# Performance work log

Hardware: AMD Instinct MI355X
Metric: run time of the kernel (lower is better)

The kernel has to match this reference:

```python
import jax, jax.numpy as jnp
import numpy as np

P, D_IN, RANK, D_OUT, N = 64, 1024, 64, 1024, 4096


def setup_inputs() -> dict:
    key = jax.random.key(0)
    k1, k2, k3, k4, k5 = jax.random.split(key, 5)
    x = jax.random.normal(k1, (N, D_IN), dtype=jnp.float32)
    pids = jax.random.randint(k2, (N,), 0, P, dtype=jnp.int64)
    U = jax.random.normal(k3, (P, D_IN, RANK), dtype=jnp.float32) * 0.02
    V = jax.random.normal(k4, (P, RANK, D_OUT), dtype=jnp.float32) * 0.02
    bias = jax.random.normal(k5, (D_OUT,), dtype=jnp.float32)
    return {"x": x, "pids": pids, "U": U, "V": V, "bias": bias}


def reference(x, pids, U, V, bias):
    # Equivalent to: for each token n, out[n] = x[n] @ U[pids[n]] @ V[pids[n]] + bias
    # Computed as dense grouped GEMM over all partitions, then row-select by pid
    # (identical math to the masked per-partition loop in the torch module).
    h = jnp.einsum('nd,pdr->pnr', x, U)        # [P, N, R]
    o = jnp.einsum('pnr,pro->pno', h, V)       # [P, N, D_out]
    out = o[pids, jnp.arange(x.shape[0])] + bias  # select each token's own partition
    return out
```

## Files before the change

kernel.cpp:

```cpp
#include <hip/hip_runtime.h>
#include <hip/hip_bf16.h>

#define NP     64
#define D_IN   1024
#define RANK   64
#define D_OUT  1024
#define NTOK   4096
#define TM     64
#define BK     64
#define MT     128
#define KS     8
#define KW     (D_IN / KS)
#define OW     128
#define LDSTR  72
#define BTH    1024

typedef __bf16 bf16x8 __attribute__((ext_vector_type(8)));
typedef float  f32x4  __attribute__((ext_vector_type(4)));

__device__ __forceinline__ unsigned short f2bf(float f) {
    unsigned u = __builtin_bit_cast(unsigned, f);
    u += 0x7FFFu + ((u >> 16) & 1u);
    return (unsigned short)(u >> 16);
}
__device__ __forceinline__ float bf2f(unsigned short s) {
    unsigned u = (unsigned)s << 16;
    return __builtin_bit_cast(float, u);
}
__device__ __forceinline__ bf16x8 pack8(float4 a, float4 b) {
    union { bf16x8 v; unsigned short s[8]; } r;
    r.s[0] = f2bf(a.x); r.s[1] = f2bf(a.y); r.s[2] = f2bf(a.z); r.s[3] = f2bf(a.w);
    r.s[4] = f2bf(b.x); r.s[5] = f2bf(b.y); r.s[6] = f2bf(b.z); r.s[7] = f2bf(b.w);
    return r.v;
}

__device__ __forceinline__ int swz_idx(int outer, int inner) {
    int blk = (inner >> 3) ^ ((outer >> 3) & 7);
    return outer * LDSTR + blk * 8 + (inner & 7);
}

__device__ __forceinline__ void decode_xcd(int b, int& tile, int& slice) {
    int g = b & 7;
    int l = b >> 3;
    slice = l >> 4;
    int m = l & 15;
    tile = (((m >> 1) << 3) | g) * 2 + (m & 1);
}

__global__ __launch_bounds__(BTH) void bucket_kernel(
    const int* __restrict__ pids, int* __restrict__ meta)
{
    __shared__ int counts[NP];
    __shared__ int cursor[NP];
    int tid = threadIdx.x;
    if (tid < NP) counts[tid] = 0;
    __syncthreads();
    for (int i = tid; i < NTOK / 4; i += BTH) {
        int4 pv = reinterpret_cast<const int4*>(pids)[i];
        atomicAdd(&counts[pv.x & (NP - 1)], 1);
        atomicAdd(&counts[pv.y & (NP - 1)], 1);
        atomicAdd(&counts[pv.z & (NP - 1)], 1);
        atomicAdd(&counts[pv.w & (NP - 1)], 1);
    }
    __syncthreads();
    if (tid < 64) {
        int c = counts[tid];
        int ntp = (c + TM - 1) >> 6;
        int sc = c, st = ntp;
        for (int d = 1; d < 64; d <<= 1) {
            int vc = __shfl_up(sc, d);
            int vt = __shfl_up(st, d);
            if (tid >= d) { sc += vc; st += vt; }
        }
        int cbase = sc - c;
        int tb    = st - ntp;
        cursor[tid] = cbase;
        for (int t = 0; t < ntp; ++t) {
            int idx = tb + t;
            int rem = c - t * TM;
            int4 rec = {tid, cbase + t * TM, rem < TM ? rem : TM, 0};
            *reinterpret_cast<int4*>(meta + 16 + 4 * idx) = rec;
        }
        if (tid == 63) meta[0] = st;
    }
    __syncthreads();
    int* bucket = meta + 1024;
    for (int i = tid; i < NTOK / 4; i += BTH) {
        int4 pv = reinterpret_cast<const int4*>(pids)[i];
        bucket[atomicAdd(&cursor[pv.x & (NP - 1)], 1)] = i * 4 + 0;
        bucket[atomicAdd(&cursor[pv.y & (NP - 1)], 1)] = i * 4 + 1;
        bucket[atomicAdd(&cursor[pv.z & (NP - 1)], 1)] = i * 4 + 2;
        bucket[atomicAdd(&cursor[pv.w & (NP - 1)], 1)] = i * 4 + 3;
    }
}

__global__ __launch_bounds__(256, 4) void h_kernel(
    const float* __restrict__ x, const float* __restrict__ U,
    const int* __restrict__ meta, unsigned short* __restrict__ Hpart)
{
    __shared__ __align__(16) unsigned short Us[2][RANK * LDSTR];

    int tile, ks;
    decode_xcd(blockIdx.x, tile, ks);
    int nt = meta[0];
    if (tile >= nt) return;
    int4 ti = *reinterpret_cast<const int4*>(meta + 16 + 4 * tile);
    int p = ti.x, off = ti.y, len = ti.z;

    int tid  = threadIdx.x;
    int lane = tid & 63;
    int w    = tid >> 6;
    int l15  = lane & 15;
    int l4   = lane >> 4;

    int myrow = w * 16 + l15;
    const int* bucket = meta + 1024;
    int t = (myrow < len) ? bucket[off + myrow] : -1;
    bool valid = (t >= 0);
    const float* xrow = x + (size_t)(valid ? t : 0) * D_IN;
    const float* Up = U + (size_t)p * D_IN * RANK;

    int kbeg = ks * KW;
    int kk = tid >> 2;
    int q  = (tid & 3) * 16;

    float4 z{0,0,0,0};
    float4 c0a=z,c0b=z,c0c=z,c0d=z,c1a=z,c1b=z,c1c=z,c1d=z;
    if (valid) {
        const float* xp = xrow + kbeg + l4 * 8;
        c0a = *reinterpret_cast<const float4*>(xp);
        c0b = *reinterpret_cast<const float4*>(xp + 4);
        c0c = *reinterpret_cast<const float4*>(xp + 32);
        c0d = *reinterpret_cast<const float4*>(xp + 36);
        c1a = *reinterpret_cast<const float4*>(xp + 64);
        c1b = *reinterpret_cast<const float4*>(xp + 68);
        c1c = *reinterpret_cast<const float4*>(xp + 96);
        c1d = *reinterpret_cast<const float4*>(xp + 100);
    }

    f32x4 acc[4] = {};

    {
        const float* up = Up + (size_t)(kbeg + kk) * RANK + q;
#pragma unroll
        for (int i = 0; i < 4; ++i) {
            float4 v = *reinterpret_cast<const float4*>(up + i * 4);
            int r = q + i * 4;
            Us[0][swz_idx(r + 0, kk)] = f2bf(v.x);
            Us[0][swz_idx(r + 1, kk)] = f2bf(v.y);
            Us[0][swz_idx(r + 2, kk)] = f2bf(v.z);
            Us[0][swz_idx(r + 3, kk)] = f2bf(v.w);
        }
    }
    __syncthreads();

    float4 u10, u11, u12, u13;
    {
        const float* up = Up + (size_t)(kbeg + BK + kk) * RANK + q;
        u10 = *reinterpret_cast<const float4*>(up);
        u11 = *reinterpret_cast<const float4*>(up + 4);
        u12 = *reinterpret_cast<const float4*>(up + 8);
        u13 = *reinterpret_cast<const float4*>(up + 12);
    }

    {
        bf16x8 a0 = pack8(c0a, c0b);
        bf16x8 a1 = pack8(c0c, c0d);
#pragma unroll
        for (int k2 = 0; k2 < 2; ++k2) {
            int kof = k2 * 32 + l4 * 8;
            bf16x8 a = k2 ? a1 : a0;
#pragma unroll
            for (int ni = 0; ni < 4; ++ni) {
                bf16x8 b = *reinterpret_cast<const bf16x8*>(&Us[0][swz_idx(ni * 16 + l15, kof)]);
                acc[ni] = __builtin_amdgcn_mfma_f32_16x16x32_bf16(a, b, acc[ni], 0, 0, 0);
            }
        }
    }

    {
        float4 vv[4] = {u10, u11, u12, u13};
#pragma unroll
        for (int i = 0; i < 4; ++i) {
            int r = q + i * 4;
            Us[1][swz_idx(r + 0, kk)] = f2bf(vv[i].x);
            Us[1][swz_idx(r + 1, kk)] = f2bf(vv[i].y);
            Us[1][swz_idx(r + 2, kk)] = f2bf(vv[i].z);
            Us[1][swz_idx(r + 3, kk)] = f2bf(vv[i].w);
        }
    }
    __syncthreads();

    {
        bf16x8 a0 = pack8(c1a, c1b);
        bf16x8 a1 = pack8(c1c, c1d);
#pragma unroll
        for (int k2 = 0; k2 < 2; ++k2) {
            int kof = k2 * 32 + l4 * 8;
            bf16x8 a = k2 ? a1 : a0;
#pragma unroll
            for (int ni = 0; ni < 4; ++ni) {
                bf16x8 b = *reinterpret_cast<const bf16x8*>(&Us[1][swz_idx(ni * 16 + l15, kof)]);
                acc[ni] = __builtin_amdgcn_mfma_f32_16x16x32_bf16(a, b, acc[ni], 0, 0, 0);
            }
        }
    }

    unsigned short* hp = Hpart + ((size_t)ks * MT + tile) * (TM * RANK);
#pragma unroll
    for (int ni = 0; ni < 4; ++ni)
#pragma unroll
        for (int j = 0; j < 4; ++j) {
            int row = w * 16 + l4 * 4 + j;
            int col = ni * 16 + l15;
            hp[row * RANK + col] = f2bf(acc[ni][j]);
        }
}

__global__ __launch_bounds__(256, 4) void o_kernel(
    const float* __restrict__ V, const float* __restrict__ bias,
    const int* __restrict__ meta, const unsigned short* __restrict__ Hpart,
    float* __restrict__ out)
{
    __shared__ __align__(16) unsigned short Vs[OW * LDSTR];

    int tile, ocs;
    decode_xcd(blockIdx.x, tile, ocs);
    int oc = ocs * OW;
    int nt = meta[0];
    if (tile >= nt) return;
    int4 ti = *reinterpret_cast<const int4*>(meta + 16 + 4 * tile);
    int p = ti.x, off = ti.y, len = ti.z;

    int tid  = threadIdx.x;
    int lane = tid & 63;
    int w    = tid >> 6;
    int l15  = lane & 15;
    int l4   = lane >> 4;

    const float* Vp = V + (size_t)p * RANK * D_OUT;
    int o4 = (tid & 31) * 4;
    int rb = tid >> 5;
    float4 vv[8];
#pragma unroll
    for (int pass = 0; pass < 8; ++pass) {
        int r = pass * 8 + rb;
        vv[pass] = *reinterpret_cast<const float4*>(&Vp[(size_t)r * D_OUT + oc + o4]);
    }

    size_t hoff = (size_t)tile * (TM * RANK) + (w * 16 + l15) * RANK + l4 * 8;
    float s0[8] = {}, s1[8] = {};
#pragma unroll
    for (int k = 0; k < KS; ++k) {
        const unsigned short* pp = Hpart + (size_t)k * (MT * TM * RANK) + hoff;
        union { int4 i4; unsigned short u[8]; } va, vb;
        va.i4 = *reinterpret_cast<const int4*>(pp);
        vb.i4 = *reinterpret_cast<const int4*>(pp + 32);
#pragma unroll
        for (int j = 0; j < 8; ++j) { s0[j] += bf2f(va.u[j]); s1[j] += bf2f(vb.u[j]); }
    }
    union { bf16x8 v; unsigned short u[8]; } fa0, fa1;
#pragma unroll
    for (int j = 0; j < 8; ++j) { fa0.u[j] = f2bf(s0[j]); fa1.u[j] = f2bf(s1[j]); }

#pragma unroll
    for (int pass = 0; pass < 8; ++pass) {
        int r = pass * 8 + rb;
        Vs[swz_idx(o4 + 0, r)] = f2bf(vv[pass].x);
        Vs[swz_idx(o4 + 1, r)] = f2bf(vv[pass].y);
        Vs[swz_idx(o4 + 2, r)] = f2bf(vv[pass].z);
        Vs[swz_idx(o4 + 3, r)] = f2bf(vv[pass].w);
    }
    __syncthreads();

    f32x4 acc[8] = {};
#pragma unroll
    for (int k2 = 0; k2 < 2; ++k2) {
        int kof = k2 * 32 + l4 * 8;
        bf16x8 a = k2 ? fa1.v : fa0.v;
#pragma unroll
        for (int ni = 0; ni < 8; ++ni) {
            bf16x8 b = *reinterpret_cast<const bf16x8*>(&Vs[swz_idx(ni * 16 + l15, kof)]);
            acc[ni] = __builtin_amdgcn_mfma_f32_16x16x32_bf16(a, b, acc[ni], 0, 0, 0);
        }
    }

    const int* bucket = meta + 1024;
    int r0 = w * 16 + l4 * 4;
    int t0 = bucket[off + r0 + 0], t1 = bucket[off + r0 + 1];
    int t2 = bucket[off + r0 + 2], t3 = bucket[off + r0 + 3];
#pragma unroll
    for (int ni = 0; ni < 8; ++ni) {
        int col = oc + ni * 16 + l15;
        float bv = bias[col];
        if (r0 + 0 < len) out[(size_t)t0 * D_OUT + col] = acc[ni][0] + bv;
        if (r0 + 1 < len) out[(size_t)t1 * D_OUT + col] = acc[ni][1] + bv;
        if (r0 + 2 < len) out[(size_t)t2 * D_OUT + col] = acc[ni][2] + bv;
        if (r0 + 3 < len) out[(size_t)t3 * D_OUT + col] = acc[ni][3] + bv;
    }
}

extern "C" void kernel_launch(void* const* d_in, const int* in_sizes, int n_in,
                              void* d_out, int out_size, void* d_ws, size_t ws_size,
                              hipStream_t stream) {
    const float* x    = (const float*)d_in[0];
    const int*   pids = (const int*)d_in[1];
    const float* U    = (const float*)d_in[2];
    const float* V    = (const float*)d_in[3];
    const float* bias = (const float*)d_in[4];
    float* out = (float*)d_out;

    int* meta = (int*)d_ws;
    unsigned short* Hpart = (unsigned short*)((char*)d_ws + 65536);

    bucket_kernel<<<1, BTH, 0, stream>>>(pids, meta);
    h_kernel<<<MT * KS, 256, 0, stream>>>(x, U, meta, Hpart);
    o_kernel<<<MT * 8, 256, 0, stream>>>(V, bias, meta, Hpart, out);
}
```

Baseline: 37.60 us.

## Fuse token bucketing into h_kernel by recomputing histogram per block

Removes the single-block bucket kernel launch and has every h_kernel block redundantly read all pids, build the partition histogram and tile prefix in LDS, then compute its own tile's token list with a stable in-block scan. The ks==0 blocks write tile records and the compacted token list to the workspace for o_kernel. It also hoists o_kernel's token index loads ahead of the reduction. This trades a serial launch and one-block kernel for redundant per-block work (4096 pids loads plus a few scan passes with barriers in each of 1024 blocks). Bucket order now lays each tile out at tile*TM rather than a contiguous per-partition offset, which is consistent because o_kernel reads the offset from the record.

```diff
diff --git a/kernel.cpp b/kernel.cpp
--- a/kernel.cpp
+++ b/kernel.cpp
@@ -13,7 +13,6 @@
 #define KW     (D_IN / KS)
 #define OW     128
 #define LDSTR  72
-#define BTH    1024
 
 typedef __bf16 bf16x8 __attribute__((ext_vector_type(8)));
 typedef float  f32x4  __attribute__((ext_vector_type(4)));
@@ -47,65 +46,18 @@
     tile = (((m >> 1) << 3) | g) * 2 + (m & 1);
 }
 
-__global__ __launch_bounds__(BTH) void bucket_kernel(
-    const int* __restrict__ pids, int* __restrict__ meta)
-{
-    __shared__ int counts[NP];
-    __shared__ int cursor[NP];
-    int tid = threadIdx.x;
-    if (tid < NP) counts[tid] = 0;
-    __syncthreads();
-    for (int i = tid; i < NTOK / 4; i += BTH) {
-        int4 pv = reinterpret_cast<const int4*>(pids)[i];
-        atomicAdd(&counts[pv.x & (NP - 1)], 1);
-        atomicAdd(&counts[pv.y & (NP - 1)], 1);
-        atomicAdd(&counts[pv.z & (NP - 1)], 1);
-        atomicAdd(&counts[pv.w & (NP - 1)], 1);
-    }
-    __syncthreads();
-    if (tid < 64) {
-        int c = counts[tid];
-        int ntp = (c + TM - 1) >> 6;
-        int sc = c, st = ntp;
-        for (int d = 1; d < 64; d <<= 1) {
-            int vc = __shfl_up(sc, d);
-            int vt = __shfl_up(st, d);
-            if (tid >= d) { sc += vc; st += vt; }
-        }
-        int cbase = sc - c;
-        int tb    = st - ntp;
-        cursor[tid] = cbase;
-        for (int t = 0; t < ntp; ++t) {
-            int idx = tb + t;
-            int rem = c - t * TM;
-            int4 rec = {tid, cbase + t * TM, rem < TM ? rem : TM, 0};
-            *reinterpret_cast<int4*>(meta + 16 + 4 * idx) = rec;
-        }
-        if (tid == 63) meta[0] = st;
-    }
-    __syncthreads();
-    int* bucket = meta + 1024;
-    for (int i = tid; i < NTOK / 4; i += BTH) {
-        int4 pv = reinterpret_cast<const int4*>(pids)[i];
-        bucket[atomicAdd(&cursor[pv.x & (NP - 1)], 1)] = i * 4 + 0;
-        bucket[atomicAdd(&cursor[pv.y & (NP - 1)], 1)] = i * 4 + 1;
-        bucket[atomicAdd(&cursor[pv.z & (NP - 1)], 1)] = i * 4 + 2;
-        bucket[atomicAdd(&cursor[pv.w & (NP - 1)], 1)] = i * 4 + 3;
-    }
-}
-
 __global__ __launch_bounds__(256, 4) void h_kernel(
-    const float* __restrict__ x, const float* __restrict__ U,
-    const int* __restrict__ meta, unsigned short* __restrict__ Hpart)
+    const float* __restrict__ x, const int* __restrict__ pids,
+    const float* __restrict__ U, int* __restrict__ meta,
+    unsigned short* __restrict__ Hpart)
 {
     __shared__ __align__(16) unsigned short Us[2][RANK * LDSTR];
-
-    int tile, ks;
-    decode_xcd(blockIdx.x, tile, ks);
-    int nt = meta[0];
-    if (tile >= nt) return;
-    int4 ti = *reinterpret_cast<const int4*>(meta + 16 + 4 * tile);
-    int p = ti.x, off = ti.y, len = ti.z;
+    __shared__ int counts[NP];
+    __shared__ int tpref[NP];
+    __shared__ int ntps[NP];
+    __shared__ int toks[TM];
+    __shared__ int wtot[4];
+    __shared__ int nt_sm, pidx_sm;
 
     int tid  = threadIdx.x;
     int lane = tid & 63;
@@ -113,9 +65,95 @@
     int l15  = lane & 15;
     int l4   = lane >> 4;
 
+    int tile, ks;
+    decode_xcd(blockIdx.x, tile, ks);
+
+    int4 pv[4];
+#pragma unroll
+    for (int c = 0; c < 4; ++c)
+        pv[c] = reinterpret_cast<const int4*>(pids)[c * 256 + tid];
+
+    if (tid < NP) { counts[tid] = 0; }
+    if (tid < TM) { toks[tid] = -1; }
+    __syncthreads();
+
+#pragma unroll
+    for (int c = 0; c < 4; ++c) {
+        atomicAdd(&counts[pv[c].x & (NP - 1)], 1);
+        atomicAdd(&counts[pv[c].y & (NP - 1)], 1);
+        atomicAdd(&counts[pv[c].z & (NP - 1)], 1);
+        atomicAdd(&counts[pv[c].w & (NP - 1)], 1);
+    }
+    __syncthreads();
+
+    if (tid < 64) {
+        int c = counts[tid];
+        int ntp = (c + TM - 1) >> 6;
+        int st = ntp;
+        for (int d = 1; d < 64; d <<= 1) {
+            int v = __shfl_up(st, d);
+            if (tid >= d) st += v;
+        }
+        tpref[tid] = st - ntp;
+        ntps[tid]  = ntp;
+        if (tid == 63) nt_sm = st;
+    }
+    __syncthreads();
+
+    int nt = nt_sm;
+    if (blockIdx.x == 0 && tid == 0) meta[0] = nt;
+    if (tile >= nt) return;
+
+    if (tid < 64) {
+        if (tpref[tid] <= tile && tile < tpref[tid] + ntps[tid]) pidx_sm = tid;
+    }
+    __syncthreads();
+    int p = pidx_sm;
+    int t_local = tile - tpref[p];
+    int lo  = t_local * TM;
+    int len = counts[p] - lo; if (len > TM) len = TM;
+
+    {
+        int running = 0;
+        for (int c = 0; c < 4 && running < lo + TM; ++c) {
+            int4 pp = pv[c];
+            int m0 = ((pp.x & (NP - 1)) == p);
+            int m1 = ((pp.y & (NP - 1)) == p);
+            int m2 = ((pp.z & (NP - 1)) == p);
+            int m3 = ((pp.w & (NP - 1)) == p);
+            int mycnt = m0 + m1 + m2 + m3;
+            int s = mycnt;
+            for (int d = 1; d < 64; d <<= 1) {
+                int v = __shfl_up(s, d);
+                if (lane >= d) s += v;
+            }
+            if (lane == 63) wtot[w] = s;
+            __syncthreads();
+            int wbase = running;
+            for (int j = 0; j < 4; ++j) if (j < w) wbase += wtot[j];
+            int r = wbase + s - mycnt;
+            int g = (c * 1024) + tid * 4;
+            if (m0) { int rel = r - lo; if (rel >= 0 && rel < TM) toks[rel] = g + 0; ++r; }
+            if (m1) { int rel = r - lo; if (rel >= 0 && rel < TM) toks[rel] = g + 1; ++r; }
+            if (m2) { int rel = r - lo; if (rel >= 0 && rel < TM) toks[rel] = g + 2; ++r; }
+            if (m3) { int rel = r - lo; if (rel >= 0 && rel < TM) toks[rel] = g + 3; ++r; }
+            int tot = wtot[0] + wtot[1] + wtot[2] + wtot[3];
+            __syncthreads();
+            running += tot;
+        }
+    }
+    __syncthreads();
+
+    if (ks == 0) {
+        if (tid < TM) meta[1024 + tile * TM + tid] = toks[tid];
+        if (tid == 0) {
+            int4 rec = {p, tile * TM, len, 0};
+            *reinterpret_cast<int4*>(meta + 16 + 4 * tile) = rec;
+        }
+    }
+
     int myrow = w * 16 + l15;
-    const int* bucket = meta + 1024;
-    int t = (myrow < len) ? bucket[off + myrow] : -1;
+    int t = toks[myrow];
     bool valid = (t >= 0);
     const float* xrow = x + (size_t)(valid ? t : 0) * D_IN;
     const float* Up = U + (size_t)p * D_IN * RANK;
@@ -248,6 +286,11 @@
         vv[pass] = *reinterpret_cast<const float4*>(&Vp[(size_t)r * D_OUT + oc + o4]);
     }
 
+    const int* bucket = meta + 1024;
+    int r0 = w * 16 + l4 * 4;
+    int t0 = bucket[off + r0 + 0], t1 = bucket[off + r0 + 1];
+    int t2 = bucket[off + r0 + 2], t3 = bucket[off + r0 + 3];
+
     size_t hoff = (size_t)tile * (TM * RANK) + (w * 16 + l15) * RANK + l4 * 8;
     float s0[8] = {}, s1[8] = {};
 #pragma unroll
@@ -285,10 +328,6 @@
         }
     }
 
-    const int* bucket = meta + 1024;
-    int r0 = w * 16 + l4 * 4;
-    int t0 = bucket[off + r0 + 0], t1 = bucket[off + r0 + 1];
-    int t2 = bucket[off + r0 + 2], t3 = bucket[off + r0 + 3];
 #pragma unroll
     for (int ni = 0; ni < 8; ++ni) {
         int col = oc + ni * 16 + l15;
@@ -313,7 +352,6 @@
     int* meta = (int*)d_ws;
     unsigned short* Hpart = (unsigned short*)((char*)d_ws + 65536);
 
-    bucket_kernel<<<1, BTH, 0, stream>>>(pids, meta);
-    h_kernel<<<MT * KS, 256, 0, stream>>>(x, U, meta, Hpart);
+    h_kernel<<<MT * KS, 256, 0, stream>>>(x, pids, U, meta, Hpart);
     o_kernel<<<MT * 8, 256, 0, stream>>>(V, bias, meta, Hpart, out);
 }
```

New measurement: 42.42 us. +12.8%, slower.
